# Performance work log

Hardware: AMD Instinct MI355X
Metric: run time of the kernel (lower is better)

The kernel has to match this reference:

```python
import jax, jax.numpy as jnp
import numpy as np

E = 8        # moe_num_experts
TOPK = 2     # moe_topk
H = 1024     # hidden_size
I = 1024     # intermediate_size
ISH = I * 2  # shared experts intermediate (intermediate_size * moe_num_shared_experts)
B, S = 2, 1024


def setup_inputs() -> dict:
    key = jax.random.key(0)
    ks = jax.random.split(key, 7)
    s = 0.02
    return {
        "hidden_states": jax.random.normal(ks[0], (B, S, H), jnp.float32),
        "w_router": jax.random.normal(ks[1], (H, E), jnp.float32) * s,
        "fc1_w": jax.random.normal(ks[2], (E, H, 2 * I), jnp.float32) * s,
        "fc2_w": jax.random.normal(ks[3], (E, I, H), jnp.float32) * s,
        "gate_w": jax.random.normal(ks[4], (H, ISH), jnp.float32) * s,
        "up_w": jax.random.normal(ks[5], (H, ISH), jnp.float32) * s,
        "down_w": jax.random.normal(ks[6], (ISH, H), jnp.float32) * s,
    }


def reference(hidden_states, w_router, fc1_w, fc2_w, gate_w, up_w, down_w):
    orig_shape = hidden_states.shape
    x = hidden_states.reshape(-1, orig_shape[-1])  # [N, H]

    # --- router: top-k + softmax over the top-k logits ---
    logits = x @ w_router                               # [N, E]
    top_logits, top_idx = jax.lax.top_k(logits, TOPK)   # [N, K]
    scores = jax.nn.softmax(top_logits, axis=-1)        # [N, K]

    # --- permute tokens so same-expert tokens are contiguous ---
    flat_idx = top_idx.reshape(-1)                      # [N*K]
    sorted_idx = jnp.argsort(flat_idx)                  # [N*K]
    permuted = x[sorted_idx // TOPK]                    # [N*K, H]
    eid = flat_idx[sorted_idx]                          # expert id per permuted slot

    # --- grouped expert SwiGLU MLP (masked per-expert GEMMs; masked rows
    #     contribute exactly zero since silu(0)*0 = 0 and 0 @ W = 0) ---
    out_perm = jnp.zeros((permuted.shape[0], orig_shape[-1]), x.dtype)
    for e in range(E):
        m = (eid == e).astype(x.dtype)[:, None]         # [N*K, 1]
        h1 = (permuted * m) @ fc1_w[e]                  # [N*K, 2I]
        proj, gate = jnp.split(h1, 2, axis=-1)
        out_perm = out_perm + (jax.nn.silu(proj) * gate) @ fc2_w[e]

    # --- unpermute and combine with router scores ---
    unperm = jnp.zeros_like(out_perm).at[sorted_idx].set(out_perm)  # [N*K, H]
    moe_out = (unperm.reshape(-1, TOPK, orig_shape[-1]) * scores[:, :, None]).sum(axis=1)
    moe_out = moe_out.reshape(orig_shape)

    # --- shared experts (LlamaMLP, SwiGLU) ---
    shared = (jax.nn.silu(hidden_states @ gate_w) * (hidden_states @ up_w)) @ down_w
    return moe_out + shared
```

## Files before the change

### kernel.cpp

```cpp
#include <hip/hip_runtime.h>
#include <cstdint>


#define E_ 8
#define H_ 1024
#define I_ 1024
#define ISH_ 2048
#define NTOK 2048

typedef unsigned short u16;
using bf16x8 = __attribute__((ext_vector_type(8))) __bf16;
using f32x4  = __attribute__((ext_vector_type(4))) float;

__device__ __forceinline__ u16 f2bf(float f) {
  union { float f; unsigned u; } v; v.f = f;
  unsigned r = v.u + 0x7fffu + ((v.u >> 16) & 1u);
  return (u16)(r >> 16);
}
__device__ __forceinline__ unsigned pk2(float lo, float hi) {
  return ((unsigned)f2bf(hi) << 16) | (unsigned)f2bf(lo);
}

typedef __attribute__((address_space(1))) const void glb_v;
typedef __attribute__((address_space(3))) void lds_v;
__device__ __forceinline__ void gl16(const void* g, void* l) {
  __builtin_amdgcn_global_load_lds((glb_v*)g, (lds_v*)l, 16, 0, 0);
}
__device__ __forceinline__ f32x4 mfma16(bf16x8 a, bf16x8 b, f32x4 c) {
  return __builtin_amdgcn_mfma_f32_16x16x32_bf16(a, b, c, 0, 0, 0);
}

__device__ __forceinline__ void router_body(const float* __restrict__ x,
                                            const float* __restrict__ wr,
                                            float* __restrict__ scores,
                                            int* __restrict__ cnt,
                                            int* __restrict__ list, int tk) {
  int lane = threadIdx.x & 63;
  const float* xr = x + (size_t)tk * H_;
  float acc[E_];
#pragma unroll
  for (int e = 0; e < E_; ++e) acc[e] = 0.f;
  int h0 = lane * 16;
#pragma unroll 4
  for (int i = 0; i < 16; ++i) {
    float xv = xr[h0 + i];
    const float* w = wr + (size_t)(h0 + i) * E_;
#pragma unroll
    for (int e = 0; e < E_; ++e) acc[e] = fmaf(xv, w[e], acc[e]);
  }
#pragma unroll
  for (int off = 32; off > 0; off >>= 1) {
#pragma unroll
    for (int e = 0; e < E_; ++e) acc[e] += __shfl_xor(acc[e], off, 64);
  }
  if (lane == 0) {
    int e0 = 0; float m0 = acc[0];
#pragma unroll
    for (int e = 1; e < E_; ++e) if (acc[e] > m0) { m0 = acc[e]; e0 = e; }
    int e1 = -1; float m1 = -1e30f;
#pragma unroll
    for (int e = 0; e < E_; ++e) if (e != e0 && acc[e] > m1) { m1 = acc[e]; e1 = e; }
    float s0 = 1.f / (1.f + __expf(m1 - m0));
    scores[tk * 2 + 0] = s0;
    scores[tk * 2 + 1] = 1.f - s0;
    int p0 = atomicAdd(&cnt[e0], 1); list[e0 * NTOK + p0] = tk * 2;
    int p1 = atomicAdd(&cnt[e1], 1); list[e1 * NTOK + p1] = tk * 2 + 1;
  }
}

__device__ __forceinline__ void wtrans2(const float* __restrict__ src,
                                        u16* __restrict__ dst, int K, int N,
                                        int kb, int nb, void* smem) {
  unsigned* lt = (unsigned*)smem;
  int t = threadIdx.x;
  int c = t & 31, k8 = t >> 5;
  int k0 = kb * 64, n0 = nb * 128;
  const float* sp = src + (size_t)(k0 + k8 * 8) * N + n0 + (c << 2);
  float v[8][4];
#pragma unroll
  for (int j2 = 0; j2 < 8; ++j2) {
    float4 f = *(const float4*)(sp + (size_t)j2 * N);
    v[j2][0] = f.x; v[j2][1] = f.y; v[j2][2] = f.z; v[j2][3] = f.w;
  }
#pragma unroll
  for (int j = 0; j < 4; ++j) {
    int nl = (c << 2) + j;
    uint4 o = make_uint4(pk2(v[0][j], v[1][j]), pk2(v[2][j], v[3][j]),
                         pk2(v[4][j], v[5][j]), pk2(v[6][j], v[7][j]));
    *(uint4*)&lt[nl * 32 + ((k8 ^ (c & 7)) << 2)] = o;
  }
  __syncthreads();
  int ktiles = K >> 5;
  u16* tb = dst + (size_t)(nb * ktiles + kb * 2) * 4096;
#pragma unroll
  for (int it = 0; it < 4; ++it) {
    int lin = it * 256 + t;
    int nl = lin >> 3, kq = lin & 7;
    uint4 o = *(const uint4*)&lt[nl * 32 + ((kq ^ ((nl >> 2) & 7)) << 2)];
    *(uint4*)(tb + (kq >> 2) * 4096 + nl * 32 + (kq & 3) * 8) = o;
  }
}


__global__ __launch_bounds__(256) void prep2_k(
    const float* __restrict__ x, const float* __restrict__ wr,
    float* __restrict__ scores, int* __restrict__ cnt, int* __restrict__ list,
    u16* __restrict__ xb,
    const float* __restrict__ fc1, const float* __restrict__ fc2,
    const float* __restrict__ gw, const float* __restrict__ uw,
    const float* __restrict__ dw,
    u16* __restrict__ fc1T, u16* __restrict__ fc2T, u16* __restrict__ gwT,
    u16* __restrict__ uwT, u16* __restrict__ dwT) {
  __shared__ __align__(16) char psm[16384];
  int bid = blockIdx.x, t = threadIdx.x;
  if (bid < 512) {
    router_body(x, wr, scores, cnt, list, bid * 4 + (t >> 6));
    return;
  }
  if (bid < 1024) {
    const float4* srcx = (const float4*)x;
    ushort4* dstx = (ushort4*)xb;
    int base = (bid - 512) * 1024 + t;
#pragma unroll
    for (int it = 0; it < 4; ++it) {
      float4 v = srcx[base + it * 256];
      ushort4 o;
      o.x = f2bf(v.x); o.y = f2bf(v.y); o.z = f2bf(v.z); o.w = f2bf(v.w);
      dstx[base + it * 256] = o;
    }
    return;
  }
  if (bid < 3072) {
    int b = bid - 1024;
    int e = b >> 8, q = b & 255;
    wtrans2(fc1 + ((size_t)e << 21), fc1T + ((size_t)e << 21), 1024, 2048,
            q & 15, q >> 4, psm);
  } else if (bid < 3328) {
    int q = bid - 3072;
    wtrans2(gw, gwT, 1024, 2048, q & 15, q >> 4, psm);
  } else if (bid < 3584) {
    int q = bid - 3328;
    wtrans2(uw, uwT, 1024, 2048, q & 15, q >> 4, psm);
  } else if (bid < 4608) {
    int b = bid - 3584;
    int e = b >> 7, q = b & 127;
    wtrans2(fc2 + ((size_t)e << 20), fc2T + ((size_t)e << 20), 1024, 1024,
            q & 15, q >> 4, psm);
  } else {
    int q = bid - 4608;
    wtrans2(dw, dwT, 2048, 1024, q & 31, q >> 5, psm);
  }
}

__global__ __launch_bounds__(256, 2) void swiglu3_k(
    const u16* __restrict__ xb, const int* __restrict__ cnt,
    const int* __restrict__ list, const u16* __restrict__ fc1T,
    const u16* __restrict__ gwT, const u16* __restrict__ uwT,
    u16* __restrict__ act, u16* __restrict__ tmp) {
  __shared__ __align__(16) u16 As[2][4096];
  __shared__ __align__(16) u16 B1s[2][4096];
  __shared__ __align__(16) u16 B2s[2][4096];

  int bid = blockIdx.x;
  int m0, n0, Me, obase = 0, ldo;
  const u16 *B1, *B2;
  const int* rowmap = nullptr;
  u16* Out;
  if (bid < 256) {
    int mb = bid >> 4, nb = bid & 15;
    m0 = mb * 128; n0 = nb * 128; Me = NTOK;
    B1 = gwT + (size_t)(nb * 32) * 4096;
    B2 = uwT + (size_t)(nb * 32) * 4096;
    Out = tmp; ldo = ISH_;
  } else {
    int b2 = bid - 256; int e = b2 >> 7, r = b2 & 127, mb = r >> 3, nb = r & 7;
    Me = cnt[e]; m0 = mb * 128;
    if (m0 >= Me) return;
    n0 = nb * 128;
    rowmap = list + e * NTOK;
    const u16* fe = fc1T + ((size_t)e << 21);
    B1 = fe + (size_t)(nb * 32) * 4096;
    B2 = fe + (size_t)((8 + nb) * 32) * 4096;
    int off = 0;
    for (int q = 0; q < e; ++q) off += cnt[q];
    obase = off; Out = act; ldo = I_;
  }
  int t = threadIdx.x, wid = t >> 6, lane = t & 63;
  int wm = wid & 1, wn = wid >> 1, lr = lane & 15, lkg = lane >> 4;
  int cq = lane & 3, crw = lane >> 2;

  const u16* arow[2];
#pragma unroll
  for (int i = 0; i < 2; ++i) {
    int c = wid * 2 + i;
    int rl = m0 + c * 16 + crw;
    int rc = rl < Me ? rl : (Me - 1);
    int tok = rowmap ? (rowmap[rc] >> 1) : rc;
    arow[i] = xb + (size_t)tok * 1024 + cq * 8;
  }

  auto stage = [&](int cb, int kt) {
#pragma unroll
    for (int i = 0; i < 2; ++i) {
      int c = wid * 2 + i;
      int bo = wid * 1024 + i * 512;
      gl16(arow[i] + kt * 32, As[cb] + c * 512);
      gl16(B1 + kt * 4096 + bo + lane * 8, B1s[cb] + bo);
      gl16(B2 + kt * 4096 + bo + lane * 8, B2s[cb] + bo);
    }
  };

  f32x4 aP[4][4] = {}, aG[4][4] = {};
  auto compute = [&](int cb) {
    bf16x8 af[4];
#pragma unroll
    for (int f = 0; f < 4; ++f)
      af[f] = *(const bf16x8*)(As[cb] + (wm * 64 + f * 16 + lr) * 32 + lkg * 8);
#pragma unroll
    for (int fn = 0; fn < 4; ++fn) {
      bf16x8 b1 = *(const bf16x8*)(B1s[cb] + (wn * 64 + fn * 16 + lr) * 32 + lkg * 8);
      bf16x8 b2 = *(const bf16x8*)(B2s[cb] + (wn * 64 + fn * 16 + lr) * 32 + lkg * 8);
#pragma unroll
      for (int fm = 0; fm < 4; ++fm) {
        aP[fm][fn] = mfma16(af[fm], b1, aP[fm][fn]);
        aG[fm][fn] = mfma16(af[fm], b2, aG[fm][fn]);
      }
    }
  };

  stage(0, 0);
  __syncthreads();
  int cur = 0;
  for (int kt = 1; kt < 32; ++kt) {
    stage(cur ^ 1, kt);
    compute(cur);
    __syncthreads();
    cur ^= 1;
  }
  compute(cur);

#pragma unroll
  for (int fm = 0; fm < 4; ++fm)
#pragma unroll
    for (int fn = 0; fn < 4; ++fn)
#pragma unroll
      for (int j = 0; j < 4; ++j) {
        int row = m0 + wm * 64 + fm * 16 + lkg * 4 + j;
        if (row < Me) {
          float p = aP[fm][fn][j], g = aG[fm][fn][j];
          float s = p / (1.f + __expf(-p)) * g;
          Out[(size_t)(obase + row) * ldo + n0 + wn * 64 + fn * 16 + lr] = f2bf(s);
        }
      }
}

__global__ __launch_bounds__(256, 2) void out3_k(
    const u16* __restrict__ act, const u16* __restrict__ fc2T,
    const u16* __restrict__ tmp, const u16* __restrict__ dwT,
    const int* __restrict__ cnt, const int* __restrict__ list,
    const float* __restrict__ scores, float* __restrict__ out) {
  __shared__ __align__(16) u16 As[2][4096];
  __shared__ __align__(16) u16 Bs[2][4096];

  int bid = blockIdx.x;
  int Me, m0, n0, lda, akoff = 0, mode, e = 0;
  const u16 *Ab, *Bt;
  const int* listE = nullptr;
  if (bid < 1024) {
    e = bid >> 7; int r = bid & 127, mb = r >> 3, nb = r & 7;
    Me = cnt[e]; m0 = mb * 128;
    if (m0 >= Me) return;
    n0 = nb * 128;
    int off = 0;
    for (int q = 0; q < e; ++q) off += cnt[q];
    Ab = act + (size_t)off * 1024; lda = 1024;
    Bt = fc2T + ((size_t)e << 20) + (size_t)(nb * 32) * 4096;
    listE = list + e * NTOK; mode = 0;
  } else {
    int r = bid - 1024, ks = r >> 7, rr = r & 127, mb = rr >> 3, nb = rr & 7;
    Me = NTOK; m0 = mb * 128; n0 = nb * 128;
    Ab = tmp; lda = 2048; akoff = ks * 1024;
    Bt = dwT + (size_t)(nb * 64 + ks * 32) * 4096;
    mode = 1;
  }
  int t = threadIdx.x, wid = t >> 6, lane = t & 63;
  int wm = wid & 1, wn = wid >> 1, lr = lane & 15, lkg = lane >> 4;
  int cq = lane & 3, crw = lane >> 2;

  const u16* arow[2];
#pragma unroll
  for (int i = 0; i < 2; ++i) {
    int c = wid * 2 + i;
    int rl = m0 + c * 16 + crw;
    int rc = rl < Me ? rl : (Me - 1);
    arow[i] = Ab + (size_t)rc * lda + akoff + cq * 8;
  }

  auto stage = [&](int cb, int kt) {
#pragma unroll
    for (int i = 0; i < 2; ++i) {
      int c = wid * 2 + i;
      int bo = wid * 1024 + i * 512;
      gl16(arow[i] + kt * 32, As[cb] + c * 512);
      gl16(Bt + kt * 4096 + bo + lane * 8, Bs[cb] + bo);
    }
  };

  f32x4 acc[4][4] = {};
  auto compute = [&](int cb) {
    bf16x8 af[4];
#pragma unroll
    for (int f = 0; f < 4; ++f)
      af[f] = *(const bf16x8*)(As[cb] + (wm * 64 + f * 16 + lr) * 32 + lkg * 8);
#pragma unroll
    for (int fn = 0; fn < 4; ++fn) {
      bf16x8 bb = *(const bf16x8*)(Bs[cb] + (wn * 64 + fn * 16 + lr) * 32 + lkg * 8);
#pragma unroll
      for (int fm = 0; fm < 4; ++fm)
        acc[fm][fn] = mfma16(af[fm], bb, acc[fm][fn]);
    }
  };

  stage(0, 0);
  __syncthreads();
  int cur = 0;
  for (int kt = 1; kt < 32; ++kt) {
    stage(cur ^ 1, kt);
    compute(cur);
    __syncthreads();
    cur ^= 1;
  }
  compute(cur);

#pragma unroll
  for (int fm = 0; fm < 4; ++fm)
#pragma unroll
    for (int fn = 0; fn < 4; ++fn)
#pragma unroll
      for (int j = 0; j < 4; ++j) {
        int row = m0 + wm * 64 + fm * 16 + lkg * 4 + j;
        if (row < Me) {
          float v = acc[fm][fn][j];
          int c = n0 + wn * 64 + fn * 16 + lr;
          if (mode == 0) {
            int slot = listE[row];
            atomicAdd(&out[(size_t)(slot >> 1) * H_ + c], v * scores[slot]);
          } else {
            atomicAdd(&out[(size_t)row * H_ + c], v);
          }
        }
      }
}

#define BM 128
#define BN 64
#define BK 32
#define PK (BK + 8)

__global__ void router_k(const float* __restrict__ x, const float* __restrict__ wr,
                         float* __restrict__ scores, int* __restrict__ cnt,
                         int* __restrict__ list) {
  int wid = threadIdx.x >> 6;
  int tk = blockIdx.x * 4 + wid;
  if (tk >= NTOK) return;
  router_body(x, wr, scores, cnt, list, tk);
}

__global__ void offs_k(const int* __restrict__ cnt, int* __restrict__ offs) {
  if (threadIdx.x == 0 && blockIdx.x == 0) {
    int s = 0;
    for (int e = 0; e < E_; ++e) { offs[e] = s; s += cnt[e]; }
  }
}

__global__ void cvt_k(const float* __restrict__ x, u16* __restrict__ xb, int n4) {
  int i = blockIdx.x * blockDim.x + threadIdx.x;
  if (i >= n4) return;
  float4 v = reinterpret_cast<const float4*>(x)[i];
  ushort4 o;
  o.x = f2bf(v.x); o.y = f2bf(v.y); o.z = f2bf(v.z); o.w = f2bf(v.w);
  reinterpret_cast<ushort4*>(xb)[i] = o;
}

template <int EXPERT>
__global__ __launch_bounds__(256) void swiglu_gemm_k(
    const u16* __restrict__ A, int lda,
    const int* __restrict__ list, const int* __restrict__ cnt, const int* __restrict__ offs,
    const float* __restrict__ B1g, const float* __restrict__ B2g, int ldb, long long bstride,
    u16* __restrict__ Out, int ldo, int K) {
  __shared__ u16 As[BM][PK];
  __shared__ u16 Bs[2][BN][PK];
  int e = EXPERT ? blockIdx.z : 0;
  int Me = EXPERT ? cnt[e] : NTOK;
  int m0 = blockIdx.y * BM;
  if (m0 >= Me) return;
  int n0 = blockIdx.x * BN;
  const int* rowmap = EXPERT ? (list + e * NTOK) : nullptr;
  const float* B1 = B1g + (EXPERT ? (long long)e * bstride : 0);
  const float* B2 = B2g + (EXPERT ? (long long)e * bstride : 0);
  int t = threadIdx.x, wid = t >> 6, lane = t & 63;
  int wm = wid & 1, wn = wid >> 1, lr = lane & 15, lkg = lane >> 4;
  f32x4 accP[4][2] = {}, accG[4][2] = {};
  for (int k0 = 0; k0 < K; k0 += BK) {
#pragma unroll
    for (int it = 0; it < 2; ++it) {
      int idx = it * 256 + t, r = idx >> 2, q = idx & 3, row = m0 + r;
      uint4 v = make_uint4(0u, 0u, 0u, 0u);
      if (row < Me) {
        int rg = EXPERT ? (rowmap[row] >> 1) : row;
        v = *reinterpret_cast<const uint4*>(A + (size_t)rg * lda + k0 + q * 8);
      }
      *reinterpret_cast<uint4*>(&As[r][q * 8]) = v;
    }
#pragma unroll
    for (int b = 0; b < 2; ++b) {
      const float* Bp = b ? B2 : B1;
#pragma unroll
      for (int it = 0; it < 2; ++it) {
        int idx = (it * 256 + t) * 4, kr = idx >> 6, c = idx & 63;
        float4 f = *reinterpret_cast<const float4*>(Bp + (size_t)(k0 + kr) * ldb + n0 + c);
        Bs[b][c + 0][kr] = f2bf(f.x); Bs[b][c + 1][kr] = f2bf(f.y);
        Bs[b][c + 2][kr] = f2bf(f.z); Bs[b][c + 3][kr] = f2bf(f.w);
      }
    }
    __syncthreads();
    bf16x8 af[4];
#pragma unroll
    for (int fm = 0; fm < 4; ++fm)
      af[fm] = *reinterpret_cast<const bf16x8*>(&As[wm * 64 + fm * 16 + lr][lkg * 8]);
#pragma unroll
    for (int fn = 0; fn < 2; ++fn) {
      bf16x8 bp = *reinterpret_cast<const bf16x8*>(&Bs[0][wn * 32 + fn * 16 + lr][lkg * 8]);
      bf16x8 bg = *reinterpret_cast<const bf16x8*>(&Bs[1][wn * 32 + fn * 16 + lr][lkg * 8]);
#pragma unroll
      for (int fm = 0; fm < 4; ++fm) {
        accP[fm][fn] = __builtin_amdgcn_mfma_f32_16x16x32_bf16(af[fm], bp, accP[fm][fn], 0, 0, 0);
        accG[fm][fn] = __builtin_amdgcn_mfma_f32_16x16x32_bf16(af[fm], bg, accG[fm][fn], 0, 0, 0);
      }
    }
    __syncthreads();
  }
#pragma unroll
  for (int fm = 0; fm < 4; ++fm)
#pragma unroll
    for (int fn = 0; fn < 2; ++fn)
#pragma unroll
      for (int j = 0; j < 4; ++j) {
        int grow = wm * 64 + fm * 16 + lkg * 4 + j, gcol = wn * 32 + fn * 16 + lr;
        int row = m0 + grow;
        if (row < Me) {
          float p = accP[fm][fn][j], g = accG[fm][fn][j];
          float s = p / (1.f + __expf(-p)) * g;
          int orow = EXPERT ? (offs[e] + row) : row;
          Out[(size_t)orow * ldo + n0 + gcol] = f2bf(s);
        }
      }
}

template <int EXPERT>
__global__ __launch_bounds__(256) void out_gemm_k(
    const u16* __restrict__ A, int lda,
    const int* __restrict__ cnt, const int* __restrict__ offs,
    const int* __restrict__ list, const float* __restrict__ scores,
    const float* __restrict__ Bg, int ldb, long long bstride,
    float* __restrict__ Out, const float* __restrict__ outbuf, int K) {
  __shared__ u16 As[BM][PK];
  __shared__ u16 Bs[BN][PK];
  int e = EXPERT ? blockIdx.z : 0;
  int Me = EXPERT ? cnt[e] : NTOK;
  int m0 = blockIdx.y * BM;
  if (m0 >= Me) return;
  int n0 = blockIdx.x * BN;
  const float* B = Bg + (EXPERT ? (long long)e * bstride : 0);
  int aoff = EXPERT ? offs[e] : 0;
  int t = threadIdx.x, wid = t >> 6, lane = t & 63;
  int wm = wid & 1, wn = wid >> 1, lr = lane & 15, lkg = lane >> 4;
  f32x4 acc[4][2] = {};
  for (int k0 = 0; k0 < K; k0 += BK) {
#pragma unroll
    for (int it = 0; it < 2; ++it) {
      int idx = it * 256 + t, r = idx >> 2, q = idx & 3, row = m0 + r;
      uint4 v = make_uint4(0u, 0u, 0u, 0u);
      if (row < Me)
        v = *reinterpret_cast<const uint4*>(A + (size_t)(aoff + row) * lda + k0 + q * 8);
      *reinterpret_cast<uint4*>(&As[r][q * 8]) = v;
    }
#pragma unroll
    for (int it = 0; it < 2; ++it) {
      int idx = (it * 256 + t) * 4, kr = idx >> 6, c = idx & 63;
      float4 f = *reinterpret_cast<const float4*>(B + (size_t)(k0 + kr) * ldb + n0 + c);
      Bs[c + 0][kr] = f2bf(f.x); Bs[c + 1][kr] = f2bf(f.y);
      Bs[c + 2][kr] = f2bf(f.z); Bs[c + 3][kr] = f2bf(f.w);
    }
    __syncthreads();
    bf16x8 af[4];
#pragma unroll
    for (int fm = 0; fm < 4; ++fm)
      af[fm] = *reinterpret_cast<const bf16x8*>(&As[wm * 64 + fm * 16 + lr][lkg * 8]);
#pragma unroll
    for (int fn = 0; fn < 2; ++fn) {
      bf16x8 bb = *reinterpret_cast<const bf16x8*>(&Bs[wn * 32 + fn * 16 + lr][lkg * 8]);
#pragma unroll
      for (int fm = 0; fm < 4; ++fm)
        acc[fm][fn] = __builtin_amdgcn_mfma_f32_16x16x32_bf16(af[fm], bb, acc[fm][fn], 0, 0, 0);
    }
    __syncthreads();
  }
#pragma unroll
  for (int fm = 0; fm < 4; ++fm)
#pragma unroll
    for (int fn = 0; fn < 2; ++fn)
#pragma unroll
      for (int j = 0; j < 4; ++j) {
        int grow = wm * 64 + fm * 16 + lkg * 4 + j, gcol = wn * 32 + fn * 16 + lr;
        int row = m0 + grow;
        if (row < Me) {
          float v = acc[fm][fn][j];
          int c = n0 + gcol;
          if (EXPERT) {
            int slot = list[e * NTOK + row];
            Out[(size_t)slot * H_ + c] = v * scores[slot];
          } else {
            Out[(size_t)row * H_ + c] =
                v + outbuf[(size_t)(2 * row) * H_ + c] + outbuf[(size_t)(2 * row + 1) * H_ + c];
          }
        }
      }
}

extern "C" void kernel_launch(void* const* d_in, const int* in_sizes, int n_in,
                              void* d_out, int out_size, void* d_ws, size_t ws_size,
                              hipStream_t stream) {
  const float* x   = (const float*)d_in[0];
  const float* wr  = (const float*)d_in[1];
  const float* fc1 = (const float*)d_in[2];
  const float* fc2 = (const float*)d_in[3];
  const float* gw  = (const float*)d_in[4];
  const float* uw  = (const float*)d_in[5];
  const float* dw  = (const float*)d_in[6];
  float* out = (float*)d_out;
  char* ws = (char*)d_ws;

  const size_t NEED_FAST = 131072ull + (88ull << 20);
  if (ws_size >= NEED_FAST) {
    float* scores = (float*)ws;
    int* cnt  = (int*)(ws + 16384);
    int* list = (int*)(ws + 16512);
    u16* xb   = (u16*)(ws + 131072);
    u16* act  = (u16*)(ws + 131072 + (4ll << 20));
    u16* tmp  = (u16*)(ws + 131072 + (12ll << 20));
    u16* fc1T = (u16*)(ws + 131072 + (28ll << 20));
    u16* fc2T = (u16*)(ws + 131072 + (60ll << 20));
    u16* gwT  = (u16*)(ws + 131072 + (76ll << 20));
    u16* uwT  = (u16*)(ws + 131072 + (80ll << 20));
    u16* dwT  = (u16*)(ws + 131072 + (84ll << 20));

    hipMemsetAsync(cnt, 0, 128, stream);
    hipMemsetAsync(out, 0, (size_t)NTOK * H_ * sizeof(float), stream);
    prep2_k<<<4864, 256, 0, stream>>>(x, wr, scores, cnt, list, xb,
                                      fc1, fc2, gw, uw, dw,
                                      fc1T, fc2T, gwT, uwT, dwT);
    swiglu3_k<<<1280, 256, 0, stream>>>(xb, cnt, list, fc1T, gwT, uwT, act, tmp);
    out3_k<<<1280, 256, 0, stream>>>(act, fc2T, tmp, dwT, cnt, list, scores, out);
  } else {
    float* scores = (float*)(ws);
    int*   cnt    = (int*)(ws + (16 << 10));
    int*   offs   = (int*)(ws + (16 << 10) + 128);
    int*   list   = (int*)(ws + (16 << 10) + 256);
    u16*   xb     = (u16*)(ws + (96 << 10));
    u16*   act    = (u16*)(ws + (96 << 10) + (4ll << 20));
    u16*   tmp    = (u16*)(ws + (96 << 10) + (12ll << 20));
    float* outbuf = (float*)(ws + (96 << 10) + (20ll << 20));

    hipMemsetAsync(cnt, 0, E_ * sizeof(int), stream);
    router_k<<<NTOK / 4, 256, 0, stream>>>(x, wr, scores, cnt, list);
    offs_k<<<1, 64, 0, stream>>>(cnt, offs);
    cvt_k<<<(NTOK * H_ / 4 + 255) / 256, 256, 0, stream>>>(x, xb, NTOK * H_ / 4);
    swiglu_gemm_k<1><<<dim3(I_ / BN, NTOK / BM, E_), 256, 0, stream>>>(
        xb, H_, list, cnt, offs, fc1, fc1 + I_, 2 * I_, (long long)H_ * 2 * I_, act, I_, H_);
    out_gemm_k<1><<<dim3(H_ / BN, NTOK / BM, E_), 256, 0, stream>>>(
        act, I_, cnt, offs, list, scores, fc2, H_, (long long)I_ * H_, outbuf, nullptr, I_);
    swiglu_gemm_k<0><<<dim3(ISH_ / BN, NTOK / BM, 1), 256, 0, stream>>>(
        xb, H_, nullptr, nullptr, nullptr, gw, uw, ISH_, 0, tmp, ISH_, H_);
    out_gemm_k<0><<<dim3(H_ / BN, NTOK / BM, 1), 256, 0, stream>>>(
        tmp, ISH_, nullptr, nullptr, nullptr, nullptr, dw, H_, 0, out, outbuf, ISH_);
  }
  (void)in_sizes; (void)n_in; (void)out_size;
}
```

Before: 267.2 us.

## Replace tiled weight transpose with k8-interleaved bf16 layout and split prep

The weight preprocessing no longer transposes fp32 weights into 32x128 K-major tiles. It converts each group of 8 K-rows into an interleaved bf16 layout ([k/8][n][8]) using a simpler LDS pass, and the GEMM kernels' B staging and LDS fragment reads are rewritten for that layout. Prep is split into two kernels, with fc2/down conversion placed after the first GEMM, so fc2's buffer can reuse fc1's workspace and the workspace requirement shrinks. The intent is cheaper weight conversion and better-coalesced writes, at the cost of strided B loads across K rows in the GEMMs and an extra kernel launch.

Measured after the change: 259.4 us. -3.0%, faster.

```diff
diff --git a/kernel.cpp b/kernel.cpp
--- a/kernel.cpp
+++ b/kernel.cpp
@@ -16,9 +16,6 @@
   union { float f; unsigned u; } v; v.f = f;
   unsigned r = v.u + 0x7fffu + ((v.u >> 16) & 1u);
   return (u16)(r >> 16);
-}
-__device__ __forceinline__ unsigned pk2(float lo, float hi) {
-  return ((unsigned)f2bf(hi) << 16) | (unsigned)f2bf(lo);
 }
 
 typedef __attribute__((address_space(1))) const void glb_v;
@@ -68,94 +65,82 @@
   }
 }
 
-__device__ __forceinline__ void wtrans2(const float* __restrict__ src,
-                                        u16* __restrict__ dst, int K, int N,
-                                        int kb, int nb, void* smem) {
-  unsigned* lt = (unsigned*)smem;
+__device__ __forceinline__ void cvt_span(const float* __restrict__ src,
+                                         u16* __restrict__ dst, int blk) {
+  size_t base = (size_t)blk * 8192 + threadIdx.x * 4;
+#pragma unroll
+  for (int i = 0; i < 8; ++i) {
+    float4 v = *(const float4*)(src + base + (size_t)i * 1024);
+    ushort4 o;
+    o.x = f2bf(v.x); o.y = f2bf(v.y); o.z = f2bf(v.z); o.w = f2bf(v.w);
+    *(ushort4*)(dst + base + (size_t)i * 1024) = o;
+  }
+}
+
+__device__ __forceinline__ void w8_span(const float* __restrict__ src,
+                                        u16* __restrict__ dst, int N, int kb,
+                                        void* smem) {
+  u16* lds = (u16*)smem;
   int t = threadIdx.x;
-  int c = t & 31, k8 = t >> 5;
-  int k0 = kb * 64, n0 = nb * 128;
-  const float* sp = src + (size_t)(k0 + k8 * 8) * N + n0 + (c << 2);
-  float v[8][4];
-#pragma unroll
-  for (int j2 = 0; j2 < 8; ++j2) {
-    float4 f = *(const float4*)(sp + (size_t)j2 * N);
-    v[j2][0] = f.x; v[j2][1] = f.y; v[j2][2] = f.z; v[j2][3] = f.w;
-  }
-#pragma unroll
-  for (int j = 0; j < 4; ++j) {
-    int nl = (c << 2) + j;
-    uint4 o = make_uint4(pk2(v[0][j], v[1][j]), pk2(v[2][j], v[3][j]),
-                         pk2(v[4][j], v[5][j]), pk2(v[6][j], v[7][j]));
-    *(uint4*)&lt[nl * 32 + ((k8 ^ (c & 7)) << 2)] = o;
+  const float* sp = src + (size_t)kb * 8 * N;
+  int total4 = 2 * N;
+  for (int i = t; i < total4; i += 256) {
+    float4 v = *(const float4*)(sp + (size_t)i * 4);
+    ushort4 o;
+    o.x = f2bf(v.x); o.y = f2bf(v.y); o.z = f2bf(v.z); o.w = f2bf(v.w);
+    *(ushort4*)(lds + (size_t)i * 4) = o;
   }
   __syncthreads();
-  int ktiles = K >> 5;
-  u16* tb = dst + (size_t)(nb * ktiles + kb * 2) * 4096;
-#pragma unroll
-  for (int it = 0; it < 4; ++it) {
-    int lin = it * 256 + t;
-    int nl = lin >> 3, kq = lin & 7;
-    uint4 o = *(const uint4*)&lt[nl * 32 + ((kq ^ ((nl >> 2) & 7)) << 2)];
-    *(uint4*)(tb + (kq >> 2) * 4096 + nl * 32 + (kq & 3) * 8) = o;
-  }
-}
-
-
-__global__ __launch_bounds__(256) void prep2_k(
+  u16* dp = dst + (size_t)kb * N * 8;
+  for (int n = t; n < N; n += 256) {
+    uint4 o;
+    o.x = (unsigned)lds[0 * N + n] | ((unsigned)lds[1 * N + n] << 16);
+    o.y = (unsigned)lds[2 * N + n] | ((unsigned)lds[3 * N + n] << 16);
+    o.z = (unsigned)lds[4 * N + n] | ((unsigned)lds[5 * N + n] << 16);
+    o.w = (unsigned)lds[6 * N + n] | ((unsigned)lds[7 * N + n] << 16);
+    *(uint4*)(dp + (size_t)n * 8) = o;
+  }
+}
+
+
+__global__ __launch_bounds__(256) void prep_a_k(
     const float* __restrict__ x, const float* __restrict__ wr,
     float* __restrict__ scores, int* __restrict__ cnt, int* __restrict__ list,
     u16* __restrict__ xb,
-    const float* __restrict__ fc1, const float* __restrict__ fc2,
-    const float* __restrict__ gw, const float* __restrict__ uw,
-    const float* __restrict__ dw,
-    u16* __restrict__ fc1T, u16* __restrict__ fc2T, u16* __restrict__ gwT,
-    u16* __restrict__ uwT, u16* __restrict__ dwT) {
-  __shared__ __align__(16) char psm[16384];
-  int bid = blockIdx.x, t = threadIdx.x;
-  if (bid < 512) {
-    router_body(x, wr, scores, cnt, list, bid * 4 + (t >> 6));
-    return;
-  }
+    const float* __restrict__ fc1, const float* __restrict__ gw,
+    const float* __restrict__ uw,
+    u16* __restrict__ fc1b, u16* __restrict__ gwb, u16* __restrict__ uwb) {
+  __shared__ __align__(16) u16 psm[8 * 2048];
+  int bid = blockIdx.x;
+  if (bid < 512) { router_body(x, wr, scores, cnt, list, bid * 4 + (threadIdx.x >> 6)); return; }
+  if (bid < 768) { cvt_span(x, xb, bid - 512); return; }
+  if (bid < 1792) {
+    int b = bid - 768, e = b >> 7, kb = b & 127;
+    w8_span(fc1 + ((size_t)e << 21), fc1b + ((size_t)e << 21), 2048, kb, psm);
+  } else if (bid < 1920) {
+    w8_span(gw, gwb, 2048, bid - 1792, psm);
+  } else {
+    w8_span(uw, uwb, 2048, bid - 1920, psm);
+  }
+}
+
+__global__ __launch_bounds__(256) void prep_b_k(
+    const float* __restrict__ fc2, const float* __restrict__ dw,
+    u16* __restrict__ fc2b, u16* __restrict__ dwb) {
+  __shared__ __align__(16) u16 psm[8 * 2048];
+  int bid = blockIdx.x;
   if (bid < 1024) {
-    const float4* srcx = (const float4*)x;
-    ushort4* dstx = (ushort4*)xb;
-    int base = (bid - 512) * 1024 + t;
-#pragma unroll
-    for (int it = 0; it < 4; ++it) {
-      float4 v = srcx[base + it * 256];
-      ushort4 o;
-      o.x = f2bf(v.x); o.y = f2bf(v.y); o.z = f2bf(v.z); o.w = f2bf(v.w);
-      dstx[base + it * 256] = o;
-    }
-    return;
-  }
-  if (bid < 3072) {
-    int b = bid - 1024;
-    int e = b >> 8, q = b & 255;
-    wtrans2(fc1 + ((size_t)e << 21), fc1T + ((size_t)e << 21), 1024, 2048,
-            q & 15, q >> 4, psm);
-  } else if (bid < 3328) {
-    int q = bid - 3072;
-    wtrans2(gw, gwT, 1024, 2048, q & 15, q >> 4, psm);
-  } else if (bid < 3584) {
-    int q = bid - 3328;
-    wtrans2(uw, uwT, 1024, 2048, q & 15, q >> 4, psm);
-  } else if (bid < 4608) {
-    int b = bid - 3584;
-    int e = b >> 7, q = b & 127;
-    wtrans2(fc2 + ((size_t)e << 20), fc2T + ((size_t)e << 20), 1024, 1024,
-            q & 15, q >> 4, psm);
+    int e = bid >> 7, kb = bid & 127;
+    w8_span(fc2 + ((size_t)e << 20), fc2b + ((size_t)e << 20), 1024, kb, psm);
   } else {
-    int q = bid - 4608;
-    wtrans2(dw, dwT, 2048, 1024, q & 31, q >> 5, psm);
-  }
-}
-
-__global__ __launch_bounds__(256, 2) void swiglu3_k(
+    w8_span(dw, dwb, 1024, bid - 1024, psm);
+  }
+}
+
+__global__ __launch_bounds__(256, 2) void swiglu5_k(
     const u16* __restrict__ xb, const int* __restrict__ cnt,
-    const int* __restrict__ list, const u16* __restrict__ fc1T,
-    const u16* __restrict__ gwT, const u16* __restrict__ uwT,
+    const int* __restrict__ list, const u16* __restrict__ fc1b,
+    const u16* __restrict__ gwb, const u16* __restrict__ uwb,
     u16* __restrict__ act, u16* __restrict__ tmp) {
   __shared__ __align__(16) u16 As[2][4096];
   __shared__ __align__(16) u16 B1s[2][4096];
@@ -169,8 +154,7 @@
   if (bid < 256) {
     int mb = bid >> 4, nb = bid & 15;
     m0 = mb * 128; n0 = nb * 128; Me = NTOK;
-    B1 = gwT + (size_t)(nb * 32) * 4096;
-    B2 = uwT + (size_t)(nb * 32) * 4096;
+    B1 = gwb + (size_t)n0 * 8; B2 = uwb + (size_t)n0 * 8;
     Out = tmp; ldo = ISH_;
   } else {
     int b2 = bid - 256; int e = b2 >> 7, r = b2 & 127, mb = r >> 3, nb = r & 7;
@@ -178,13 +162,14 @@
     if (m0 >= Me) return;
     n0 = nb * 128;
     rowmap = list + e * NTOK;
-    const u16* fe = fc1T + ((size_t)e << 21);
-    B1 = fe + (size_t)(nb * 32) * 4096;
-    B2 = fe + (size_t)((8 + nb) * 32) * 4096;
+    const u16* fe = fc1b + ((size_t)e << 21);
+    B1 = fe + (size_t)n0 * 8;
+    B2 = fe + (size_t)(1024 + n0) * 8;
     int off = 0;
     for (int q = 0; q < e; ++q) off += cnt[q];
     obase = off; Out = act; ldo = I_;
   }
+  const int ldn = 2048;
   int t = threadIdx.x, wid = t >> 6, lane = t & 63;
   int wm = wid & 1, wn = wid >> 1, lr = lane & 15, lkg = lane >> 4;
   int cq = lane & 3, crw = lane >> 2;
@@ -198,15 +183,18 @@
     int tok = rowmap ? (rowmap[rc] >> 1) : rc;
     arow[i] = xb + (size_t)tok * 1024 + cq * 8;
   }
+  const u16* b1base = B1 + ((size_t)wid * ldn + lane) * 8;
+  const u16* b2base = B2 + ((size_t)wid * ldn + lane) * 8;
 
   auto stage = [&](int cb, int kt) {
-#pragma unroll
-    for (int i = 0; i < 2; ++i) {
-      int c = wid * 2 + i;
-      int bo = wid * 1024 + i * 512;
-      gl16(arow[i] + kt * 32, As[cb] + c * 512);
-      gl16(B1 + kt * 4096 + bo + lane * 8, B1s[cb] + bo);
-      gl16(B2 + kt * 4096 + bo + lane * 8, B2s[cb] + bo);
+    size_t ko = (size_t)kt * 4 * ldn * 8;
+#pragma unroll
+    for (int i = 0; i < 2; ++i)
+      gl16(arow[i] + kt * 32, As[cb] + (wid * 2 + i) * 512);
+#pragma unroll
+    for (int h = 0; h < 2; ++h) {
+      gl16(b1base + ko + h * 64 * 8, B1s[cb] + wid * 1024 + h * 512);
+      gl16(b2base + ko + h * 64 * 8, B2s[cb] + wid * 1024 + h * 512);
     }
   };
 
@@ -218,8 +206,9 @@
       af[f] = *(const bf16x8*)(As[cb] + (wm * 64 + f * 16 + lr) * 32 + lkg * 8);
 #pragma unroll
     for (int fn = 0; fn < 4; ++fn) {
-      bf16x8 b1 = *(const bf16x8*)(B1s[cb] + (wn * 64 + fn * 16 + lr) * 32 + lkg * 8);
-      bf16x8 b2 = *(const bf16x8*)(B2s[cb] + (wn * 64 + fn * 16 + lr) * 32 + lkg * 8);
+      int col = wn * 64 + fn * 16 + lr;
+      bf16x8 b1 = *(const bf16x8*)(B1s[cb] + lkg * 1024 + col * 8);
+      bf16x8 b2 = *(const bf16x8*)(B2s[cb] + lkg * 1024 + col * 8);
 #pragma unroll
       for (int fm = 0; fm < 4; ++fm) {
         aP[fm][fn] = mfma16(af[fm], b1, aP[fm][fn]);
@@ -254,9 +243,9 @@
       }
 }
 
-__global__ __launch_bounds__(256, 2) void out3_k(
-    const u16* __restrict__ act, const u16* __restrict__ fc2T,
-    const u16* __restrict__ tmp, const u16* __restrict__ dwT,
+__global__ __launch_bounds__(256, 2) void out5_k(
+    const u16* __restrict__ act, const u16* __restrict__ fc2b,
+    const u16* __restrict__ tmp, const u16* __restrict__ dwb,
     const int* __restrict__ cnt, const int* __restrict__ list,
     const float* __restrict__ scores, float* __restrict__ out) {
   __shared__ __align__(16) u16 As[2][4096];
@@ -264,7 +253,7 @@
 
   int bid = blockIdx.x;
   int Me, m0, n0, lda, akoff = 0, mode, e = 0;
-  const u16 *Ab, *Bt;
+  const u16 *Ab, *Bn;
   const int* listE = nullptr;
   if (bid < 1024) {
     e = bid >> 7; int r = bid & 127, mb = r >> 3, nb = r & 7;
@@ -274,15 +263,16 @@
     int off = 0;
     for (int q = 0; q < e; ++q) off += cnt[q];
     Ab = act + (size_t)off * 1024; lda = 1024;
-    Bt = fc2T + ((size_t)e << 20) + (size_t)(nb * 32) * 4096;
+    Bn = fc2b + ((size_t)e << 20) + (size_t)n0 * 8;
     listE = list + e * NTOK; mode = 0;
   } else {
     int r = bid - 1024, ks = r >> 7, rr = r & 127, mb = rr >> 3, nb = rr & 7;
     Me = NTOK; m0 = mb * 128; n0 = nb * 128;
     Ab = tmp; lda = 2048; akoff = ks * 1024;
-    Bt = dwT + (size_t)(nb * 64 + ks * 32) * 4096;
+    Bn = dwb + ((size_t)ks * 128 * 1024 + n0) * 8;
     mode = 1;
   }
+  const int ldn = 1024;
   int t = threadIdx.x, wid = t >> 6, lane = t & 63;
   int wm = wid & 1, wn = wid >> 1, lr = lane & 15, lkg = lane >> 4;
   int cq = lane & 3, crw = lane >> 2;
@@ -295,15 +285,16 @@
     int rc = rl < Me ? rl : (Me - 1);
     arow[i] = Ab + (size_t)rc * lda + akoff + cq * 8;
   }
+  const u16* bbase = Bn + ((size_t)wid * ldn + lane) * 8;
 
   auto stage = [&](int cb, int kt) {
-#pragma unroll
-    for (int i = 0; i < 2; ++i) {
-      int c = wid * 2 + i;
-      int bo = wid * 1024 + i * 512;
-      gl16(arow[i] + kt * 32, As[cb] + c * 512);
-      gl16(Bt + kt * 4096 + bo + lane * 8, Bs[cb] + bo);
-    }
+    size_t ko = (size_t)kt * 4 * ldn * 8;
+#pragma unroll
+    for (int i = 0; i < 2; ++i)
+      gl16(arow[i] + kt * 32, As[cb] + (wid * 2 + i) * 512);
+#pragma unroll
+    for (int h = 0; h < 2; ++h)
+      gl16(bbase + ko + h * 64 * 8, Bs[cb] + wid * 1024 + h * 512);
   };
 
   f32x4 acc[4][4] = {};
@@ -314,7 +305,8 @@
       af[f] = *(const bf16x8*)(As[cb] + (wm * 64 + f * 16 + lr) * 32 + lkg * 8);
 #pragma unroll
     for (int fn = 0; fn < 4; ++fn) {
-      bf16x8 bb = *(const bf16x8*)(Bs[cb] + (wn * 64 + fn * 16 + lr) * 32 + lkg * 8);
+      int col = wn * 64 + fn * 16 + lr;
+      bf16x8 bb = *(const bf16x8*)(Bs[cb] + lkg * 1024 + col * 8);
 #pragma unroll
       for (int fm = 0; fm < 4; ++fm)
         acc[fm][fn] = mfma16(af[fm], bb, acc[fm][fn]);
@@ -541,7 +533,7 @@
   float* out = (float*)d_out;
   char* ws = (char*)d_ws;
 
-  const size_t NEED_FAST = 131072ull + (88ull << 20);
+  const size_t NEED_FAST = 131072ull + (68ull << 20);
   if (ws_size >= NEED_FAST) {
     float* scores = (float*)ws;
     int* cnt  = (int*)(ws + 16384);
@@ -549,19 +541,19 @@
     u16* xb   = (u16*)(ws + 131072);
     u16* act  = (u16*)(ws + 131072 + (4ll << 20));
     u16* tmp  = (u16*)(ws + 131072 + (12ll << 20));
-    u16* fc1T = (u16*)(ws + 131072 + (28ll << 20));
-    u16* fc2T = (u16*)(ws + 131072 + (60ll << 20));
-    u16* gwT  = (u16*)(ws + 131072 + (76ll << 20));
-    u16* uwT  = (u16*)(ws + 131072 + (80ll << 20));
-    u16* dwT  = (u16*)(ws + 131072 + (84ll << 20));
+    u16* fc1b = (u16*)(ws + 131072 + (20ll << 20));
+    u16* gwb  = (u16*)(ws + 131072 + (52ll << 20));
+    u16* uwb  = (u16*)(ws + 131072 + (60ll << 20));
+    u16* fc2b = fc1b;
+    u16* dwb  = (u16*)(ws + 131072 + (36ll << 20));
 
     hipMemsetAsync(cnt, 0, 128, stream);
     hipMemsetAsync(out, 0, (size_t)NTOK * H_ * sizeof(float), stream);
-    prep2_k<<<4864, 256, 0, stream>>>(x, wr, scores, cnt, list, xb,
-                                      fc1, fc2, gw, uw, dw,
-                                      fc1T, fc2T, gwT, uwT, dwT);
-    swiglu3_k<<<1280, 256, 0, stream>>>(xb, cnt, list, fc1T, gwT, uwT, act, tmp);
-    out3_k<<<1280, 256, 0, stream>>>(act, fc2T, tmp, dwT, cnt, list, scores, out);
+    prep_a_k<<<2048, 256, 0, stream>>>(x, wr, scores, cnt, list, xb,
+                                       fc1, gw, uw, fc1b, gwb, uwb);
+    swiglu5_k<<<1280, 256, 0, stream>>>(xb, cnt, list, fc1b, gwb, uwb, act, tmp);
+    prep_b_k<<<1280, 256, 0, stream>>>(fc2, dw, fc2b, dwb);
+    out5_k<<<1280, 256, 0, stream>>>(act, fc2b, tmp, dwb, cnt, list, scores, out);
   } else {
     float* scores = (float*)(ws);
     int*   cnt    = (int*)(ws + (16 << 10));
```
